# Kernel optimization log

Hardware: AMD Instinct MI355X
Metric: run time of the kernel (lower is better)

The kernel has to match this reference:

```python
import jax, jax.numpy as jnp
import numpy as np

TAU = 1.0
TOPK = 10
VERY_NEG = -1e9


def setup_inputs() -> dict:
    key = jax.random.key(0)
    k1, k2 = jax.random.split(key)
    B, C = 4096, 32000
    z_g = jax.random.normal(k1, (B, C), dtype=jnp.float32) * 4.0
    y = jax.random.randint(k2, (B,), 0, C, dtype=jnp.int32)
    return {"z_g": z_g, "y": y}


def reference(z_g, y):
    # z_g: [B, C] teacher logits, y: [B] int labels
    B, C = z_g.shape
    dtype = z_g.dtype
    classes = jnp.arange(C, dtype=y.dtype)
    mask_nt = classes[None, :] != y[:, None]                  # [B, C] non-true mask

    # ---- topk non-true: keep top-K non-true logits, flatten the rest ----
    K = min(TOPK, C - 1)
    z_nt_only = jnp.where(mask_nt, z_g, VERY_NEG)             # true logit suppressed
    _, topi = jax.lax.top_k(z_nt_only, K)                     # [B, K]
    keep_mask = jnp.zeros((B, C), dtype=bool)
    keep_mask = keep_mask.at[jnp.arange(B)[:, None], topi].set(True)
    keep_mask = keep_mask & mask_nt
    rest_mask = mask_nt & (~keep_mask)

    # log-sum-exp over the "rest" (non-true, non-topk) logits
    z_rest = jnp.where(rest_mask, z_g, VERY_NEG)
    logS_rest = jax.nn.logsumexp(z_rest, axis=1)              # [B]
    MR = jnp.maximum(jnp.asarray(C - 1 - K, dtype), jnp.asarray(1.0, dtype))
    alphaK = logS_rest - jnp.log(MR)                          # log-mean-exp of rest
    z_nt_mod = jnp.where(rest_mask, alphaK[:, None], z_g)     # [B, C]

    # ---- set true logit to per-sample minimum v ----
    v_per = jnp.min(z_g, axis=1)                              # [B]
    z_virt = z_nt_mod.at[jnp.arange(B), y].set(v_per)

    # ---- virtual teacher distribution ----
    p_virt = jax.nn.softmax(z_virt / jnp.asarray(TAU, dtype), axis=1)
    return p_virt
```

## Files before the change

### kernel.cpp

```cpp
#include <hip/hip_runtime.h>
#include <math.h>

#define TPB 256
#define NW (TPB / 64)
#define CAP 256
#define KTOP 10
#define TCAND 11.0f

typedef float floatx4 __attribute__((ext_vector_type(4)));
typedef unsigned long long u64;
typedef unsigned int u32;

__device__ inline float wredMin(float v) {
#pragma unroll
  for (int o = 32; o >= 1; o >>= 1) v = fminf(v, __shfl_xor(v, o));
  return v;
}
__device__ inline float wredSum(float v) {
#pragma unroll
  for (int o = 32; o >= 1; o >>= 1) v += __shfl_xor(v, o);
  return v;
}
__device__ inline u64 shfl_xor_u64(u64 k, int o) {
  int lo = __shfl_xor((int)(u32)k, o);
  int hi = __shfl_xor((int)(u32)(k >> 32), o);
  return ((u64)(u32)hi << 32) | (u32)lo;
}
__device__ inline u64 wredMaxU64(u64 k) {
#pragma unroll
  for (int o = 32; o >= 1; o >>= 1) {
    u64 ok = shfl_xor_u64(k, o);
    if (ok > k) k = ok;
  }
  return k;
}
__device__ inline u64 mkkey(float z, int idx) {
  u32 b = __float_as_uint(z);
  u32 u = (b & 0x80000000u) ? ~b : (b | 0x80000000u);
  return ((u64)u << 32) | (u32)~(u32)idx;
}
__device__ inline int keyidx(u64 k) { return (int)~(u32)k; }
__device__ inline float keyval(u64 k) {
  u32 u = (u32)(k >> 32);
  u32 b = (u & 0x80000000u) ? (u ^ 0x80000000u) : ~u;
  return __uint_as_float(b);
}

struct SM {
  u64 pool[CAP];
  u64 warr[NW];
  u64 selArr[KTOP];
  float rmn[NW], rsm[NW];
  int cnt;
  float c_prest, c_ptrue;
  float pk[KTOP];
  int ki[KTOP];
};

__global__ __launch_bounds__(TPB) void fused(
    const float* __restrict__ zg, const int* __restrict__ yv,
    float* __restrict__ out, int B, int C) {
  __shared__ SM S;

  const int tid = threadIdx.x, wid = tid >> 6, lane = tid & 63;
  const int row = blockIdx.x;
  const float* zr = zg + (size_t)row * C;
  const floatx4* zr4 = (const floatx4*)zr;
  const int C4 = C >> 2;
  const int y = yv[row];
  const int Keff = KTOP < (C - 1) ? KTOP : (C - 1);

  float zy0 = 0.0f;
  if (tid == 0) { S.cnt = 0; zy0 = zr[y]; }
  __syncthreads();

  float lmin = INFINITY, lsum = 0.0f;
  for (int base = 0; base < C4; base += 4 * TPB) {
    const int q0 = base + tid, q1 = q0 + TPB, q2 = q1 + TPB, q3 = q2 + TPB;
    const bool h0 = q0 < C4, h1 = q1 < C4, h2 = q2 < C4, h3 = q3 < C4;
    floatx4 x0 = {0, 0, 0, 0}, x1 = {0, 0, 0, 0}, x2 = {0, 0, 0, 0}, x3 = {0, 0, 0, 0};
    if (h0) x0 = __builtin_nontemporal_load(zr4 + q0);
    if (h1) x1 = __builtin_nontemporal_load(zr4 + q1);
    if (h2) x2 = __builtin_nontemporal_load(zr4 + q2);
    if (h3) x3 = __builtin_nontemporal_load(zr4 + q3);
#define PROC(X, H, Q)                                                                        \
    if (H) {                                                                                 \
      lmin = fminf(lmin, fminf(fminf(X.x, X.y), fminf(X.z, X.w)));                           \
      lsum += __expf(X.x) + __expf(X.y) + __expf(X.z) + __expf(X.w);                         \
      if (fmaxf(fmaxf(X.x, X.y), fmaxf(X.z, X.w)) > TCAND) {                                 \
        int j = (Q) << 2;                                                                    \
        if (X.x > TCAND && j + 0 != y) { int p = atomicAdd(&S.cnt, 1); if (p < CAP) S.pool[p] = mkkey(X.x, j); }     \
        if (X.y > TCAND && j + 1 != y) { int p = atomicAdd(&S.cnt, 1); if (p < CAP) S.pool[p] = mkkey(X.y, j + 1); } \
        if (X.z > TCAND && j + 2 != y) { int p = atomicAdd(&S.cnt, 1); if (p < CAP) S.pool[p] = mkkey(X.z, j + 2); } \
        if (X.w > TCAND && j + 3 != y) { int p = atomicAdd(&S.cnt, 1); if (p < CAP) S.pool[p] = mkkey(X.w, j + 3); } \
      }                                                                                      \
    }
    PROC(x0, h0, q0) PROC(x1, h1, q1) PROC(x2, h2, q2) PROC(x3, h3, q3)
#undef PROC
  }
  for (int j = (C4 << 2) + tid; j < C; j += TPB) {
    float z = zr[j];
    lmin = fminf(lmin, z);
    lsum += __expf(z);
    if (z > TCAND && j != y) { int p = atomicAdd(&S.cnt, 1); if (p < CAP) S.pool[p] = mkkey(z, j); }
  }

  lmin = wredMin(lmin);
  lsum = wredSum(lsum);
  if (lane == 0) { S.rmn[wid] = lmin; S.rsm[wid] = lsum; }
  __syncthreads();

  const int pc = S.cnt;
  float vmin = INFINITY, total = 0.0f;
#pragma unroll
  for (int w = 0; w < NW; ++w) { vmin = fminf(vmin, S.rmn[w]); total += S.rsm[w]; }
  const bool ok = (pc >= Keff && pc <= CAP);

  if (ok) {
    if (wid == 0) {
      u64 s0 = (lane < pc)       ? S.pool[lane]       : 0;
      u64 s1 = (lane + 64 < pc)  ? S.pool[lane + 64]  : 0;
      u64 s2 = (lane + 128 < pc) ? S.pool[lane + 128] : 0;
      u64 s3 = (lane + 192 < pc) ? S.pool[lane + 192] : 0;
      u64 sel[KTOP];
      u64 prev = ~0ull;
#pragma unroll
      for (int r = 0; r < KTOP; ++r) {
        u64 loc = 0;
        if (r < Keff) {
          if (s0 < prev && s0 > loc) loc = s0;
          if (s1 < prev && s1 > loc) loc = s1;
          if (s2 < prev && s2 > loc) loc = s2;
          if (s3 < prev && s3 > loc) loc = s3;
        }
        u64 best = wredMaxU64(loc);
        sel[r] = best;
        prev = best;
      }
      if (lane == 0) {
        float Stop = 0.0f;
#pragma unroll
        for (int r = 0; r < KTOP; ++r)
          if (sel[r] != 0) Stop += __expf(keyval(sel[r]));
        const float Sall = total - __expf(zy0);
        const float ev   = __expf(vmin);
        const float invZ = 1.0f / (Sall + ev);
        float Srest = Sall - Stop;
        if (Srest < 0.0f) Srest = 0.0f;
        float MR = (float)(C - 1 - Keff);
        if (MR < 1.0f) MR = 1.0f;
        S.c_prest = (Srest / MR) * invZ;
        S.c_ptrue = ev * invZ;
#pragma unroll
        for (int r = 0; r < KTOP; ++r) {
          bool have = (sel[r] != 0);
          S.pk[r] = have ? __expf(keyval(sel[r])) * invZ : 0.0f;
          S.ki[r] = have ? keyidx(sel[r]) : -1;
        }
      }
    }
  } else {
    u64 prev = ~0ull;
    for (int r = 0; r < KTOP; ++r) {
      u64 loc = 0;
      if (r < Keff) {
        for (int j = tid; j < C; j += TPB) {
          if (j == y) continue;
          u64 k = mkkey(zr[j], j);
          if (k < prev && k > loc) loc = k;
        }
      }
      u64 best = wredMaxU64(loc);
      if (lane == 0) S.warr[wid] = best;
      __syncthreads();
      if (tid == 0) {
        u64 b = 0;
#pragma unroll
        for (int w = 0; w < NW; ++w) b = (S.warr[w] > b) ? S.warr[w] : b;
        S.selArr[r] = b;
      }
      __syncthreads();
      prev = S.selArr[r];
    }
    if (tid == 0) {
      float Stop = 0.0f;
#pragma unroll
      for (int r = 0; r < KTOP; ++r)
        if (S.selArr[r] != 0) Stop += __expf(keyval(S.selArr[r]));
      const float Sall = total - __expf(zy0);
      const float ev   = __expf(vmin);
      const float invZ = 1.0f / (Sall + ev);
      float Srest = Sall - Stop;
      if (Srest < 0.0f) Srest = 0.0f;
      float MR = (float)(C - 1 - Keff);
      if (MR < 1.0f) MR = 1.0f;
      S.c_prest = (Srest / MR) * invZ;
      S.c_ptrue = ev * invZ;
#pragma unroll
      for (int r = 0; r < KTOP; ++r) {
        bool have = (S.selArr[r] != 0);
        S.pk[r] = have ? __expf(keyval(S.selArr[r])) * invZ : 0.0f;
        S.ki[r] = have ? keyidx(S.selArr[r]) : -1;
      }
    }
  }
  __syncthreads();

  const float p_rest = S.c_prest;
  const float p_true = S.c_ptrue;
  float pk[KTOP]; int ki[KTOP]; int sv[KTOP];
#pragma unroll
  for (int k = 0; k < KTOP; ++k) {
    pk[k] = S.pk[k];
    ki[k] = S.ki[k];
    sv[k] = ki[k] >> 2;
  }
  const int svy = y >> 2;

  float* orow = out + (size_t)row * C;
  floatx4* out4 = (floatx4*)orow;
  const floatx4 fillv = {p_rest, p_rest, p_rest, p_rest};
  for (int base = 0; base < C4; base += 4 * TPB) {
#pragma unroll
    for (int u = 0; u < 4; ++u) {
      int g = base + tid + u * TPB;
      if (g < C4) {
        floatx4 o = fillv;
        bool sp = (g == svy);
#pragma unroll
        for (int k = 0; k < KTOP; ++k) sp |= (g == sv[k]);
        if (sp) {
          int j = g << 2;
#pragma unroll
          for (int l = 0; l < 4; ++l) {
            float p = p_rest;
#pragma unroll
            for (int k = 0; k < KTOP; ++k)
              if (j + l == ki[k]) p = pk[k];
            if (j + l == y) p = p_true;
            o[l] = p;
          }
        }
        __builtin_nontemporal_store(o, &out4[g]);
      }
    }
  }
  for (int j = (C4 << 2) + tid; j < C; j += TPB) {
    float p = p_rest;
#pragma unroll
    for (int k = 0; k < KTOP; ++k)
      if (j == ki[k]) p = pk[k];
    if (j == y) p = p_true;
    __builtin_nontemporal_store(p, &orow[j]);
  }
}

extern "C" void kernel_launch(void* const* d_in, const int* in_sizes, int n_in,
                              void* d_out, int out_size, void* d_ws, size_t ws_size,
                              hipStream_t stream) {
  const float* zg = (const float*)d_in[0];
  const int* y    = (const int*)d_in[1];
  float* out      = (float*)d_out;
  const int B = in_sizes[1];
  const int C = in_sizes[0] / B;

  fused<<<B, TPB, 0, stream>>>(zg, y, out, B, C);
}
```

Before: 201.6 us.

## Software-pipeline rows in persistent blocks, overlapping next-row reads with previous-row writes

The kernel becomes persistent: a grid of up to 1024 blocks loops over rows with stride gridDim. In each iteration it streams in and reduces the next row while writing the output of the previous row, so loads and stores overlap within one block. This aims to keep read and write bandwidth busy at the same time, where before each block read its row fully and then wrote it. In exchange it adds extra barriers, raises register pressure, and runs fewer blocks, which may lower occupancy.

```diff
diff --git a/kernel.cpp b/kernel.cpp
--- a/kernel.cpp
+++ b/kernel.cpp
@@ -6,6 +6,7 @@
 #define CAP 256
 #define KTOP 10
 #define TCAND 11.0f
+#define NBLK 1024
 
 typedef float floatx4 __attribute__((ext_vector_type(4)));
 typedef unsigned long long u64;
@@ -52,6 +53,7 @@
   u64 selArr[KTOP];
   float rmn[NW], rsm[NW];
   int cnt;
+  float zy;
   float c_prest, c_ptrue;
   float pk[KTOP];
   int ki[KTOP];
@@ -61,197 +63,215 @@
     const float* __restrict__ zg, const int* __restrict__ yv,
     float* __restrict__ out, int B, int C) {
   __shared__ SM S;
-
   const int tid = threadIdx.x, wid = tid >> 6, lane = tid & 63;
-  const int row = blockIdx.x;
-  const float* zr = zg + (size_t)row * C;
-  const floatx4* zr4 = (const floatx4*)zr;
   const int C4 = C >> 2;
-  const int y = yv[row];
   const int Keff = KTOP < (C - 1) ? KTOP : (C - 1);
-
-  float zy0 = 0.0f;
-  if (tid == 0) { S.cnt = 0; zy0 = zr[y]; }
-  __syncthreads();
-
-  float lmin = INFINITY, lsum = 0.0f;
-  for (int base = 0; base < C4; base += 4 * TPB) {
-    const int q0 = base + tid, q1 = q0 + TPB, q2 = q1 + TPB, q3 = q2 + TPB;
-    const bool h0 = q0 < C4, h1 = q1 < C4, h2 = q2 < C4, h3 = q3 < C4;
-    floatx4 x0 = {0, 0, 0, 0}, x1 = {0, 0, 0, 0}, x2 = {0, 0, 0, 0}, x3 = {0, 0, 0, 0};
-    if (h0) x0 = __builtin_nontemporal_load(zr4 + q0);
-    if (h1) x1 = __builtin_nontemporal_load(zr4 + q1);
-    if (h2) x2 = __builtin_nontemporal_load(zr4 + q2);
-    if (h3) x3 = __builtin_nontemporal_load(zr4 + q3);
+  const int myrow0 = blockIdx.x;
+  const int NB = gridDim.x;
+  if (myrow0 >= B) return;
+  const int nrows = (B - myrow0 + NB - 1) / NB;
+
+  float p_rest = 0.0f, p_true = 0.0f;
+  float pk[KTOP];
+  int ki[KTOP], sv[KTOP];
+  int y_w = 0, svy = -2;
+#pragma unroll
+  for (int k = 0; k < KTOP; ++k) { pk[k] = 0; ki[k] = -1; sv[k] = -1; }
+
+  for (int it = 0; it <= nrows; ++it) {
+    const bool doR = (it < nrows);
+    const bool doW = (it >= 1);
+    const int rrow = myrow0 + it * NB;
+    const int wrow = myrow0 + (it - 1) * NB;
+    const float* zr = zg + (size_t)rrow * C;
+    const floatx4* zr4 = (const floatx4*)zr;
+    float* orow = out + (size_t)wrow * C;
+    floatx4* out4 = (floatx4*)orow;
+
+    __syncthreads();
+    if (doW) {
+      p_rest = S.c_prest; p_true = S.c_ptrue;
+#pragma unroll
+      for (int k = 0; k < KTOP; ++k) { pk[k] = S.pk[k]; ki[k] = S.ki[k]; sv[k] = ki[k] >> 2; }
+      y_w = yv[wrow]; svy = y_w >> 2;
+    }
+    int y_r = 0;
+    if (doR) y_r = yv[rrow];
+    if (doR && tid == 0) { S.cnt = 0; S.zy = zr[y_r]; }
+    __syncthreads();
+
+    float lmin = INFINITY, lsum = 0.0f;
+    const floatx4 fillv = {p_rest, p_rest, p_rest, p_rest};
+    for (int base = 0; base < C4; base += 4 * TPB) {
+      const int q0 = base + tid, q1 = q0 + TPB, q2 = q1 + TPB, q3 = q2 + TPB;
+      floatx4 x0 = {0, 0, 0, 0}, x1 = {0, 0, 0, 0}, x2 = {0, 0, 0, 0}, x3 = {0, 0, 0, 0};
+      bool h0 = false, h1 = false, h2 = false, h3 = false;
+      if (doR) {
+        h0 = q0 < C4; h1 = q1 < C4; h2 = q2 < C4; h3 = q3 < C4;
+        if (h0) x0 = __builtin_nontemporal_load(zr4 + q0);
+        if (h1) x1 = __builtin_nontemporal_load(zr4 + q1);
+        if (h2) x2 = __builtin_nontemporal_load(zr4 + q2);
+        if (h3) x3 = __builtin_nontemporal_load(zr4 + q3);
+      }
+      if (doW) {
+#pragma unroll
+        for (int u = 0; u < 4; ++u) {
+          int g = base + tid + u * TPB;
+          if (g < C4) {
+            floatx4 o = fillv;
+            bool sp = (g == svy);
+#pragma unroll
+            for (int k = 0; k < KTOP; ++k) sp |= (g == sv[k]);
+            if (sp) {
+              int j = g << 2;
+#pragma unroll
+              for (int l = 0; l < 4; ++l) {
+                float p = p_rest;
+#pragma unroll
+                for (int k = 0; k < KTOP; ++k)
+                  if (j + l == ki[k]) p = pk[k];
+                if (j + l == y_w) p = p_true;
+                o[l] = p;
+              }
+            }
+            __builtin_nontemporal_store(o, &out4[g]);
+          }
+        }
+      }
 #define PROC(X, H, Q)                                                                        \
-    if (H) {                                                                                 \
-      lmin = fminf(lmin, fminf(fminf(X.x, X.y), fminf(X.z, X.w)));                           \
-      lsum += __expf(X.x) + __expf(X.y) + __expf(X.z) + __expf(X.w);                         \
-      if (fmaxf(fmaxf(X.x, X.y), fmaxf(X.z, X.w)) > TCAND) {                                 \
-        int j = (Q) << 2;                                                                    \
-        if (X.x > TCAND && j + 0 != y) { int p = atomicAdd(&S.cnt, 1); if (p < CAP) S.pool[p] = mkkey(X.x, j); }     \
-        if (X.y > TCAND && j + 1 != y) { int p = atomicAdd(&S.cnt, 1); if (p < CAP) S.pool[p] = mkkey(X.y, j + 1); } \
-        if (X.z > TCAND && j + 2 != y) { int p = atomicAdd(&S.cnt, 1); if (p < CAP) S.pool[p] = mkkey(X.z, j + 2); } \
-        if (X.w > TCAND && j + 3 != y) { int p = atomicAdd(&S.cnt, 1); if (p < CAP) S.pool[p] = mkkey(X.w, j + 3); } \
-      }                                                                                      \
-    }
-    PROC(x0, h0, q0) PROC(x1, h1, q1) PROC(x2, h2, q2) PROC(x3, h3, q3)
+      if (H) {                                                                               \
+        lmin = fminf(lmin, fminf(fminf(X.x, X.y), fminf(X.z, X.w)));                         \
+        lsum += __expf(X.x) + __expf(X.y) + __expf(X.z) + __expf(X.w);                       \
+        if (fmaxf(fmaxf(X.x, X.y), fmaxf(X.z, X.w)) > TCAND) {                               \
+          int j = (Q) << 2;                                                                  \
+          if (X.x > TCAND && j + 0 != y_r) { int p = atomicAdd(&S.cnt, 1); if (p < CAP) S.pool[p] = mkkey(X.x, j); }     \
+          if (X.y > TCAND && j + 1 != y_r) { int p = atomicAdd(&S.cnt, 1); if (p < CAP) S.pool[p] = mkkey(X.y, j + 1); } \
+          if (X.z > TCAND && j + 2 != y_r) { int p = atomicAdd(&S.cnt, 1); if (p < CAP) S.pool[p] = mkkey(X.z, j + 2); } \
+          if (X.w > TCAND && j + 3 != y_r) { int p = atomicAdd(&S.cnt, 1); if (p < CAP) S.pool[p] = mkkey(X.w, j + 3); } \
+        }                                                                                    \
+      }
+      PROC(x0, h0, q0) PROC(x1, h1, q1) PROC(x2, h2, q2) PROC(x3, h3, q3)
 #undef PROC
-  }
-  for (int j = (C4 << 2) + tid; j < C; j += TPB) {
-    float z = zr[j];
-    lmin = fminf(lmin, z);
-    lsum += __expf(z);
-    if (z > TCAND && j != y) { int p = atomicAdd(&S.cnt, 1); if (p < CAP) S.pool[p] = mkkey(z, j); }
-  }
-
-  lmin = wredMin(lmin);
-  lsum = wredSum(lsum);
-  if (lane == 0) { S.rmn[wid] = lmin; S.rsm[wid] = lsum; }
-  __syncthreads();
-
-  const int pc = S.cnt;
-  float vmin = INFINITY, total = 0.0f;
-#pragma unroll
-  for (int w = 0; w < NW; ++w) { vmin = fminf(vmin, S.rmn[w]); total += S.rsm[w]; }
-  const bool ok = (pc >= Keff && pc <= CAP);
-
-  if (ok) {
-    if (wid == 0) {
-      u64 s0 = (lane < pc)       ? S.pool[lane]       : 0;
-      u64 s1 = (lane + 64 < pc)  ? S.pool[lane + 64]  : 0;
-      u64 s2 = (lane + 128 < pc) ? S.pool[lane + 128] : 0;
-      u64 s3 = (lane + 192 < pc) ? S.pool[lane + 192] : 0;
-      u64 sel[KTOP];
-      u64 prev = ~0ull;
-#pragma unroll
-      for (int r = 0; r < KTOP; ++r) {
-        u64 loc = 0;
-        if (r < Keff) {
-          if (s0 < prev && s0 > loc) loc = s0;
-          if (s1 < prev && s1 > loc) loc = s1;
-          if (s2 < prev && s2 > loc) loc = s2;
-          if (s3 < prev && s3 > loc) loc = s3;
-        }
-        u64 best = wredMaxU64(loc);
-        sel[r] = best;
-        prev = best;
-      }
-      if (lane == 0) {
-        float Stop = 0.0f;
-#pragma unroll
-        for (int r = 0; r < KTOP; ++r)
-          if (sel[r] != 0) Stop += __expf(keyval(sel[r]));
-        const float Sall = total - __expf(zy0);
-        const float ev   = __expf(vmin);
-        const float invZ = 1.0f / (Sall + ev);
-        float Srest = Sall - Stop;
-        if (Srest < 0.0f) Srest = 0.0f;
-        float MR = (float)(C - 1 - Keff);
-        if (MR < 1.0f) MR = 1.0f;
-        S.c_prest = (Srest / MR) * invZ;
-        S.c_ptrue = ev * invZ;
-#pragma unroll
+    }
+    if (doR) {
+      for (int j = (C4 << 2) + tid; j < C; j += TPB) {
+        float z = zr[j];
+        lmin = fminf(lmin, z);
+        lsum += __expf(z);
+        if (z > TCAND && j != y_r) { int p = atomicAdd(&S.cnt, 1); if (p < CAP) S.pool[p] = mkkey(z, j); }
+      }
+    }
+    if (doW) {
+      for (int j = (C4 << 2) + tid; j < C; j += TPB) {
+        float p = p_rest;
+#pragma unroll
+        for (int k = 0; k < KTOP; ++k)
+          if (j == ki[k]) p = pk[k];
+        if (j == y_w) p = p_true;
+        __builtin_nontemporal_store(p, &orow[j]);
+      }
+    }
+
+    if (doR) {
+      lmin = wredMin(lmin);
+      lsum = wredSum(lsum);
+      if (lane == 0) { S.rmn[wid] = lmin; S.rsm[wid] = lsum; }
+      __syncthreads();
+      const int pc = S.cnt;
+      float vmin = INFINITY, total = 0.0f;
+#pragma unroll
+      for (int w = 0; w < NW; ++w) { vmin = fminf(vmin, S.rmn[w]); total += S.rsm[w]; }
+      const bool ok = (pc >= Keff && pc <= CAP);
+
+      if (ok) {
+        if (wid == 0) {
+          u64 s0 = (lane < pc)       ? S.pool[lane]       : 0;
+          u64 s1 = (lane + 64 < pc)  ? S.pool[lane + 64]  : 0;
+          u64 s2 = (lane + 128 < pc) ? S.pool[lane + 128] : 0;
+          u64 s3 = (lane + 192 < pc) ? S.pool[lane + 192] : 0;
+          u64 sel[KTOP];
+          u64 prev = ~0ull;
+#pragma unroll
+          for (int r = 0; r < KTOP; ++r) {
+            u64 loc = 0;
+            if (r < Keff) {
+              if (s0 < prev && s0 > loc) loc = s0;
+              if (s1 < prev && s1 > loc) loc = s1;
+              if (s2 < prev && s2 > loc) loc = s2;
+              if (s3 < prev && s3 > loc) loc = s3;
+            }
+            u64 best = wredMaxU64(loc);
+            sel[r] = best;
+            prev = best;
+          }
+          if (lane == 0) {
+            float Stop = 0.0f;
+#pragma unroll
+            for (int r = 0; r < KTOP; ++r)
+              if (sel[r] != 0) Stop += __expf(keyval(sel[r]));
+            const float Sall = total - __expf(S.zy);
+            const float ev   = __expf(vmin);
+            const float invZ = 1.0f / (Sall + ev);
+            float Srest = Sall - Stop;
+            if (Srest < 0.0f) Srest = 0.0f;
+            float MR = (float)(C - 1 - Keff);
+            if (MR < 1.0f) MR = 1.0f;
+            S.c_prest = (Srest / MR) * invZ;
+            S.c_ptrue = ev * invZ;
+#pragma unroll
+            for (int r = 0; r < KTOP; ++r) {
+              bool have = (sel[r] != 0);
+              S.pk[r] = have ? __expf(keyval(sel[r])) * invZ : 0.0f;
+              S.ki[r] = have ? keyidx(sel[r]) : -1;
+            }
+          }
+        }
+      } else {
+        u64 prev = ~0ull;
         for (int r = 0; r < KTOP; ++r) {
-          bool have = (sel[r] != 0);
-          S.pk[r] = have ? __expf(keyval(sel[r])) * invZ : 0.0f;
-          S.ki[r] = have ? keyidx(sel[r]) : -1;
-        }
-      }
-    }
-  } else {
-    u64 prev = ~0ull;
-    for (int r = 0; r < KTOP; ++r) {
-      u64 loc = 0;
-      if (r < Keff) {
-        for (int j = tid; j < C; j += TPB) {
-          if (j == y) continue;
-          u64 k = mkkey(zr[j], j);
-          if (k < prev && k > loc) loc = k;
-        }
-      }
-      u64 best = wredMaxU64(loc);
-      if (lane == 0) S.warr[wid] = best;
-      __syncthreads();
-      if (tid == 0) {
-        u64 b = 0;
-#pragma unroll
-        for (int w = 0; w < NW; ++w) b = (S.warr[w] > b) ? S.warr[w] : b;
-        S.selArr[r] = b;
-      }
-      __syncthreads();
-      prev = S.selArr[r];
-    }
-    if (tid == 0) {
-      float Stop = 0.0f;
-#pragma unroll
-      for (int r = 0; r < KTOP; ++r)
-        if (S.selArr[r] != 0) Stop += __expf(keyval(S.selArr[r]));
-      const float Sall = total - __expf(zy0);
-      const float ev   = __expf(vmin);
-      const float invZ = 1.0f / (Sall + ev);
-      float Srest = Sall - Stop;
-      if (Srest < 0.0f) Srest = 0.0f;
-      float MR = (float)(C - 1 - Keff);
-      if (MR < 1.0f) MR = 1.0f;
-      S.c_prest = (Srest / MR) * invZ;
-      S.c_ptrue = ev * invZ;
-#pragma unroll
-      for (int r = 0; r < KTOP; ++r) {
-        bool have = (S.selArr[r] != 0);
-        S.pk[r] = have ? __expf(keyval(S.selArr[r])) * invZ : 0.0f;
-        S.ki[r] = have ? keyidx(S.selArr[r]) : -1;
-      }
-    }
-  }
-  __syncthreads();
-
-  const float p_rest = S.c_prest;
-  const float p_true = S.c_ptrue;
-  float pk[KTOP]; int ki[KTOP]; int sv[KTOP];
-#pragma unroll
-  for (int k = 0; k < KTOP; ++k) {
-    pk[k] = S.pk[k];
-    ki[k] = S.ki[k];
-    sv[k] = ki[k] >> 2;
-  }
-  const int svy = y >> 2;
-
-  float* orow = out + (size_t)row * C;
-  floatx4* out4 = (floatx4*)orow;
-  const floatx4 fillv = {p_rest, p_rest, p_rest, p_rest};
-  for (int base = 0; base < C4; base += 4 * TPB) {
-#pragma unroll
-    for (int u = 0; u < 4; ++u) {
-      int g = base + tid + u * TPB;
-      if (g < C4) {
-        floatx4 o = fillv;
-        bool sp = (g == svy);
-#pragma unroll
-        for (int k = 0; k < KTOP; ++k) sp |= (g == sv[k]);
-        if (sp) {
-          int j = g << 2;
-#pragma unroll
-          for (int l = 0; l < 4; ++l) {
-            float p = p_rest;
-#pragma unroll
-            for (int k = 0; k < KTOP; ++k)
-              if (j + l == ki[k]) p = pk[k];
-            if (j + l == y) p = p_true;
-            o[l] = p;
-          }
-        }
-        __builtin_nontemporal_store(o, &out4[g]);
-      }
-    }
-  }
-  for (int j = (C4 << 2) + tid; j < C; j += TPB) {
-    float p = p_rest;
-#pragma unroll
-    for (int k = 0; k < KTOP; ++k)
-      if (j == ki[k]) p = pk[k];
-    if (j == y) p = p_true;
-    __builtin_nontemporal_store(p, &orow[j]);
+          u64 loc = 0;
+          if (r < Keff) {
+            for (int j = tid; j < C; j += TPB) {
+              if (j == y_r) continue;
+              u64 k = mkkey(zr[j], j);
+              if (k < prev && k > loc) loc = k;
+            }
+          }
+          u64 best = wredMaxU64(loc);
+          if (lane == 0) S.warr[wid] = best;
+          __syncthreads();
+          if (tid == 0) {
+            u64 b = 0;
+#pragma unroll
+            for (int w = 0; w < NW; ++w) b = (S.warr[w] > b) ? S.warr[w] : b;
+            S.selArr[r] = b;
+          }
+          __syncthreads();
+          prev = S.selArr[r];
+        }
+        if (tid == 0) {
+          float Stop = 0.0f;
+#pragma unroll
+          for (int r = 0; r < KTOP; ++r)
+            if (S.selArr[r] != 0) Stop += __expf(keyval(S.selArr[r]));
+          const float Sall = total - __expf(S.zy);
+          const float ev   = __expf(vmin);
+          const float invZ = 1.0f / (Sall + ev);
+          float Srest = Sall - Stop;
+          if (Srest < 0.0f) Srest = 0.0f;
+          float MR = (float)(C - 1 - Keff);
+          if (MR < 1.0f) MR = 1.0f;
+          S.c_prest = (Srest / MR) * invZ;
+          S.c_ptrue = ev * invZ;
+#pragma unroll
+          for (int r = 0; r < KTOP; ++r) {
+            bool have = (S.selArr[r] != 0);
+            S.pk[r] = have ? __expf(keyval(S.selArr[r])) * invZ : 0.0f;
+            S.ki[r] = have ? keyidx(S.selArr[r]) : -1;
+          }
+        }
+      }
+    }
   }
 }
 
@@ -264,5 +284,6 @@
   const int B = in_sizes[1];
   const int C = in_sizes[0] / B;
 
-  fused<<<B, TPB, 0, stream>>>(zg, y, out, B, C);
-}
+  int nb = NBLK < B ? NBLK : B;
+  fused<<<nb, TPB, 0, stream>>>(zg, y, out, B, C);
+}
```

Result: slower. 211.4 us (+4.8%).
